# Kernel tuning notes

Hardware: AMD Instinct MI355X
Metric: run time of the kernel (lower is better)

The kernel has to match this reference:

```python
import jax, jax.numpy as jnp
import numpy as np


def cross_scan(x):
    # x: (B, D, H, W) -> xs: (B, 8, D, L)  (row, col, rev-row, rev-col, diag, antidiag, rev-diag, rev-antidiag)
    B, D, H, W = x.shape
    L = H * W
    hs = jnp.arange(H)[:, None]
    ws = jnp.arange(W)[None, :]
    x0 = x.reshape(B, D, L)                          # row-major
    x1 = jnp.swapaxes(x, 2, 3).reshape(B, D, L)      # column-major
    gd = x[:, :, hs, (hs + ws) % W]                  # diagonal gather (B,D,H,W)
    ga = x[:, :, hs, (ws - hs) % W]                  # antidiagonal gather
    x4 = jnp.swapaxes(gd, -1, -2).reshape(B, D, L)
    x5 = jnp.swapaxes(ga, -1, -2).reshape(B, D, L)
    return jnp.stack([x0, x1, x0[..., ::-1], x1[..., ::-1],
                      x4, x5, x4[..., ::-1], x5[..., ::-1]], axis=1)


def cross_merge(ys, H, W):
    # ys: (B, 8, D, L) -> (B, D, L), inverse-scatter + sum of all 8 directions
    B, K, D, L = ys.shape
    hs = jnp.arange(H)[:, None]
    ws = jnp.arange(W)[None, :]
    y = ys[:, 0] + ys[:, 2, :, ::-1]
    yt = (ys[:, 1] + ys[:, 3, :, ::-1]).reshape(B, D, W, H)
    y = y + jnp.swapaxes(yt, -1, -2).reshape(B, D, L)
    # diagonal scatter: result[h, w'] = t[h, (w'-h) % W]
    td = jnp.swapaxes((ys[:, 4] + ys[:, 6, :, ::-1]).reshape(B, D, W, H), -1, -2)
    y = y + td[:, :, hs, (ws - hs) % W].reshape(B, D, L)
    # antidiagonal scatter: result[h, w'] = t[h, (w'+h) % W]
    ta = jnp.swapaxes((ys[:, 5] + ys[:, 7, :, ::-1]).reshape(B, D, W, H), -1, -2)
    y = y + ta[:, :, hs, (ws + hs) % W].reshape(B, D, L)
    return y


def selective_scan(u, delta, A, Bs, Cs, Ds):
    # u, delta: (B, KD, L); A: (KD, N); Bs, Cs: (B, K, N, L); Ds: (KD,)
    Bb, KD, L = u.shape
    K = Bs.shape[1]
    Dh = KD // K
    N = A.shape[1]
    u_ = jnp.moveaxis(u.reshape(Bb, K, Dh, L), -1, 0)        # (L,B,K,Dh)
    d_ = jnp.moveaxis(delta.reshape(Bb, K, Dh, L), -1, 0)
    B_ = jnp.moveaxis(Bs, -1, 0)                              # (L,B,K,N)
    C_ = jnp.moveaxis(Cs, -1, 0)
    A_ = A.reshape(K, Dh, N)

    def step(h, inp):
        u_t, d_t, b_t, c_t = inp
        dA = jnp.exp(d_t[..., None] * A_)                     # (B,K,Dh,N)
        h = h * dA + (d_t * u_t)[..., None] * b_t[:, :, None, :]
        y = jnp.einsum('bkdn,bkn->bkd', h, c_t)
        return h, y

    h0 = jnp.zeros((Bb, K, Dh, N), u.dtype)
    _, ys = jax.lax.scan(step, h0, (u_, d_, B_, C_))          # ys: (L,B,K,Dh)
    ys = jnp.moveaxis(ys, 0, -1).reshape(Bb, KD, L)
    return ys + u * Ds[None, :, None]


def setup_inputs() -> dict:
    key = jax.random.key(0)
    ks = jax.random.split(key, 6)
    B, D, H, W = 2, 192, 64, 64
    K, N, R = 8, 16, 6
    x = jax.random.normal(ks[0], (B, D, H, W), jnp.float32)
    x_proj_weight = jax.random.normal(ks[1], (K, R + 2 * N, D), jnp.float32) * (1.0 / np.sqrt(D))
    dt_projs_weight = jax.random.normal(ks[2], (K, D, R), jnp.float32) * (0.1 / np.sqrt(R))
    dt_projs_bias = jax.random.normal(ks[3], (K, D), jnp.float32) * 0.1
    A_logs = jax.random.uniform(ks[4], (K * D, N), jnp.float32)
    Ds = jax.random.normal(ks[5], (K * D,), jnp.float32)
    ln_w = jnp.ones((D,), jnp.float32)
    ln_b = jnp.zeros((D,), jnp.float32)
    return {"x": x, "x_proj_weight": x_proj_weight, "dt_projs_weight": dt_projs_weight,
            "dt_projs_bias": dt_projs_bias, "A_logs": A_logs, "Ds": Ds,
            "ln_w": ln_w, "ln_b": ln_b}


def reference(x, x_proj_weight, dt_projs_weight, dt_projs_bias, A_logs, Ds, ln_w, ln_b):
    B, D, H, W = x.shape
    K = x_proj_weight.shape[0]
    N = A_logs.shape[1]
    R = dt_projs_weight.shape[2]
    L = H * W
    xs = cross_scan(x)                                            # (B,K,D,L)
    x_dbl = jnp.einsum('bkdl,kcd->bkcl', xs, x_proj_weight)       # (B,K,R+2N,L)
    dts, Bs, Cs = jnp.split(x_dbl, [R, R + N], axis=2)
    dts = jnp.einsum('bkrl,kdr->bkdl', dts, dt_projs_weight)      # (B,K,D,L)
    u = xs.reshape(B, K * D, L)
    delta = jax.nn.softplus(dts.reshape(B, K * D, L) + dt_projs_bias.reshape(1, K * D, 1))
    A = -jnp.exp(A_logs)                                          # (KD,N)
    ys = selective_scan(u, delta, A, Bs, Cs, Ds)                  # (B,KD,L)
    y = cross_merge(ys.reshape(B, K, D, L), H, W)                 # (B,D,L)
    y = jnp.swapaxes(y, 1, 2)                                     # (B,L,D)
    mu = y.mean(-1, keepdims=True)
    var = y.var(-1, keepdims=True)
    y = (y - mu) / jnp.sqrt(var + 1e-5) * ln_w + ln_b             # out_norm (LayerNorm)
    return y.reshape(B, H, W, D)
```

## Files before the change

kernel.cpp:

```cpp
#include <hip/hip_runtime.h>
#include <math.h>

#define BB   2
#define DD   192
#define LL   4096
#define KK   8
#define NN   16
#define RR   6
#define C38  38
#define CPAD 40
#define PQS  17
#define NCH  64
#define CLEN (LL / NCH)

__device__ __forceinline__ float fexp2(float x) { return __builtin_amdgcn_exp2f(x); }
__device__ __forceinline__ float flog2(float x) { return __builtin_amdgcn_logf(x); }

__device__ __forceinline__ float softplus_f(float x) {
  return fmaxf(x, 0.f) + 0.69314718f * flog2(1.f + fexp2(-1.44269504f * fabsf(x)));
}

__device__ __forceinline__ int src_index(int k, int l) {
  int ll = (k & 2) ? (LL - 1 - l) : l;
  int kb = k & 5;
  if (kb == 0) return ll;
  int h = ll & 63, w = ll >> 6;
  if (kb == 1) return (h << 6) + w;
  if (kb == 4) return (h << 6) + ((h + w) & 63);
  return (h << 6) + ((w - h) & 63);
}

__global__ __launch_bounds__(256) void transpose_x(const float* __restrict__ x,
                                                   float* __restrict__ xT) {
  __shared__ float tile[32][33];
  int b  = blockIdx.z;
  int p0 = blockIdx.x * 32;
  int d0 = blockIdx.y * 32;
  int tx = threadIdx.x, ty = threadIdx.y;
  #pragma unroll
  for (int i = 0; i < 32; i += 8)
    tile[ty + i][tx] = x[((size_t)(b * DD + d0 + ty + i)) * LL + p0 + tx];
  __syncthreads();
  #pragma unroll
  for (int i = 0; i < 32; i += 8)
    xT[((size_t)(b * LL + p0 + ty + i)) * DD + d0 + tx] = tile[tx][ty + i];
}

__global__ __launch_bounds__(256) void proj_kernel(const float* __restrict__ xT,
                                                   const float* __restrict__ W,
                                                   float* __restrict__ xdbl) {
  int k = blockIdx.y, b = blockIdx.z;
  int tx = threadIdx.x;
  int lloc = tx & 127, half = tx >> 7;
  int l = blockIdx.x * 128 + lloc;
  __shared__ __align__(16) float sm[DD * CPAD];
  for (int i = tx; i < C38 * DD; i += 256) {
    int c = i / DD, dq = i - c * DD;
    sm[dq * CPAD + c] = W[(k * C38 + c) * DD + dq];
  }
  for (int dq = tx; dq < DD; dq += 256) { sm[dq * CPAD + 38] = 0.f; sm[dq * CPAD + 39] = 0.f; }
  __syncthreads();

  int p = src_index(k, l);
  const float4* xrow4 = (const float4*)(xT + ((size_t)b * LL + p) * DD) + half * 24;
  const float* wbase = sm + half * 96 * CPAD;
  float4 acc[10];
  #pragma unroll
  for (int c = 0; c < 10; ++c) acc[c] = make_float4(0.f, 0.f, 0.f, 0.f);

  for (int d4 = 0; d4 < 24; ++d4) {
    float4 xv = xrow4[d4];
    #pragma unroll
    for (int s = 0; s < 4; ++s) {
      float xs = (s == 0) ? xv.x : (s == 1) ? xv.y : (s == 2) ? xv.z : xv.w;
      const float4* w4 = (const float4*)(wbase + (d4 * 4 + s) * CPAD);
      #pragma unroll
      for (int c = 0; c < 10; ++c) {
        float4 wv = w4[c];
        acc[c].x = fmaf(wv.x, xs, acc[c].x);
        acc[c].y = fmaf(wv.y, xs, acc[c].y);
        acc[c].z = fmaf(wv.z, xs, acc[c].z);
        acc[c].w = fmaf(wv.w, xs, acc[c].w);
      }
    }
  }
  __syncthreads();
  if (half == 1) {
    float* pr = sm + lloc * 41;
    const float* af = (const float*)acc;
    #pragma unroll
    for (int c = 0; c < 38; ++c) pr[c] = af[c];
  }
  __syncthreads();
  if (half == 0) {
    const float* pr = sm + lloc * 41;
    float* af = (float*)acc;
    #pragma unroll
    for (int c = 0; c < 38; ++c) af[c] += pr[c];
    float* orow = xdbl + ((size_t)((b * KK + k) * LL) + l) * CPAD;
    float4* o4 = (float4*)orow;
    #pragma unroll
    for (int c = 0; c < 9; ++c) o4[c] = acc[c];
    orow[36] = acc[9].x;
    orow[37] = acc[9].y;
  }
}

template <bool FINAL>
__global__ __launch_bounds__(384, 5) void scan_kernel(
    const float* __restrict__ xT, const float* __restrict__ xdbl,
    const float* __restrict__ A_logs, const float* __restrict__ dtw,
    const float* __restrict__ dtb, const float* __restrict__ Ds,
    float* __restrict__ Pq, float* __restrict__ Y) {
  const int lane = threadIdx.x;
  const int ng   = lane >> 5;
  const int dd   = threadIdx.y;
  const int bk   = blockIdx.x;
  const int chunk = blockIdx.y;
  const int b = bk >> 3, k = bk & 7;
  const int d  = dd * 32 + (lane & 31);
  const int kd = k * DD + d;
  const int ch = bk * DD + d;

  float An2[8];
  {
    const float* ap = A_logs + (size_t)kd * NN + ng * 8;
    #pragma unroll
    for (int j = 0; j < 8; ++j) An2[j] = -__expf(ap[j]) * 1.44269504f;
  }
  float wdt[RR];
  #pragma unroll
  for (int r = 0; r < RR; ++r) wdt[r] = dtw[kd * RR + r];
  const float bias = dtb[kd];
  const float dval = FINAL ? Ds[kd] : 0.f;

  float h[8];
  if constexpr (FINAL) {
    const float* h0p = Pq + ((size_t)ch * NCH + chunk) * PQS + 1 + ng * 8;
    #pragma unroll
    for (int j = 0; j < 8; ++j) h[j] = h0p[j];
  } else {
    #pragma unroll
    for (int j = 0; j < 8; ++j) h[j] = 0.f;
  }

  const int l0 = chunk * CLEN;
  const float* rowbase = xdbl + ((size_t)(bk * LL) + l0) * CPAD;
  const float* xTb = xT + (size_t)b * LL * DD + d;

  float S = 0.f;
  float sp[2], uu[2], Bv[2][8], Cv[2][8];
  int   pp[2];

  auto LOADT = [&](int t, int s) {
    const float* row = rowbase + (size_t)t * CPAD;
    const float2* r2 = (const float2*)row;
    float2 d01 = r2[0], d23 = r2[1], d45 = r2[2];
    float dts = bias;
    dts = fmaf(d01.x, wdt[0], dts);
    dts = fmaf(d01.y, wdt[1], dts);
    dts = fmaf(d23.x, wdt[2], dts);
    dts = fmaf(d23.y, wdt[3], dts);
    dts = fmaf(d45.x, wdt[4], dts);
    dts = fmaf(d45.y, wdt[5], dts);
    sp[s] = softplus_f(dts);
    const float2* bq = (const float2*)(row + 6 + ng * 8);
    #pragma unroll
    for (int j = 0; j < 4; ++j) {
      float2 v = bq[j];
      Bv[s][2 * j] = v.x; Bv[s][2 * j + 1] = v.y;
    }
    if constexpr (FINAL) {
      const float2* cq = (const float2*)(row + 22 + ng * 8);
      #pragma unroll
      for (int j = 0; j < 4; ++j) {
        float2 v = cq[j];
        Cv[s][2 * j] = v.x; Cv[s][2 * j + 1] = v.y;
      }
    }
    int p = src_index(k, l0 + t);
    pp[s] = p;
    uu[s] = xTb[(size_t)p * DD];
  };

  auto COMPUTE = [&](int s) {
    float spv = sp[s];
    float du = spv * uu[s];
    #pragma unroll
    for (int j = 0; j < 8; ++j) {
      float e = fexp2(spv * An2[j]);
      h[j] = fmaf(h[j], e, du * Bv[s][j]);
    }
    if constexpr (FINAL) {
      float y = 0.f;
      #pragma unroll
      for (int j = 0; j < 8; ++j) y = fmaf(h[j], Cv[s][j], y);
      y += __shfl_xor(y, 32, 64);
      if (ng == 0) {
        float outv = fmaf(uu[s], dval, y);
        atomicAdd(&Y[(size_t)(b * LL + pp[s]) * DD + d], outv);
      }
    } else {
      S += spv;
    }
  };

  LOADT(0, 0);
  for (int t = 0; t < CLEN; t += 2) {
    LOADT(t + 1, 1);
    COMPUTE(0);
    int t2 = (t + 2 < CLEN) ? t + 2 : CLEN - 1;
    LOADT(t2, 0);
    COMPUTE(1);
  }

  if constexpr (!FINAL) {
    float* rec = Pq + ((size_t)ch * NCH + chunk) * PQS;
    if (ng == 0) rec[0] = S;
    float* qp = rec + 1 + ng * 8;
    #pragma unroll
    for (int j = 0; j < 8; ++j) qp[j] = h[j];
  }
}

__global__ __launch_bounds__(256) void stitch_kernel(float* __restrict__ Pq,
                                                     const float* __restrict__ A_logs) {
  int lane = threadIdx.x & 63;
  int gw = (blockIdx.x * 256 + threadIdx.x) >> 6;
  int ch = gw >> 4, n = gw & 15;
  int kd = ch % (KK * DD);
  float An2 = -__expf(A_logs[(size_t)kd * NN + n]) * 1.44269504f;

  float* rec = Pq + ((size_t)ch * NCH + lane) * PQS;
  float P = fexp2(An2 * rec[0]);
  float q = rec[1 + n];

  float Pt = P, qt = q;
  #pragma unroll
  for (int off = 1; off < 64; off <<= 1) {
    float Pp = __shfl_up(Pt, off, 64);
    float qp = __shfl_up(qt, off, 64);
    if (lane >= off) { qt = fmaf(Pt, qp, qt); Pt *= Pp; }
  }
  float hx = __shfl_up(qt, 1, 64);
  if (lane == 0) hx = 0.f;
  rec[1 + n] = hx;
}

__global__ __launch_bounds__(256) void ln_kernel(const float* __restrict__ Y,
                                                 const float* __restrict__ lw,
                                                 const float* __restrict__ lb,
                                                 float* __restrict__ out) {
  int lane = threadIdx.x & 63;
  int row = blockIdx.x * 4 + (threadIdx.x >> 6);
  const float* yr = Y + (size_t)row * DD;
  float v0 = yr[lane], v1 = yr[lane + 64], v2 = yr[lane + 128];
  float s1 = v0 + v1 + v2;
  float s2 = v0 * v0 + v1 * v1 + v2 * v2;
  #pragma unroll
  for (int m = 32; m >= 1; m >>= 1) {
    s1 += __shfl_xor(s1, m, 64);
    s2 += __shfl_xor(s2, m, 64);
  }
  float mu = s1 * (1.f / DD);
  float var = s2 * (1.f / DD) - mu * mu;
  float inv = rsqrtf(var + 1e-5f);
  float* orow = out + (size_t)row * DD;
  orow[lane]       = (v0 - mu) * inv * lw[lane]       + lb[lane];
  orow[lane + 64]  = (v1 - mu) * inv * lw[lane + 64]  + lb[lane + 64];
  orow[lane + 128] = (v2 - mu) * inv * lw[lane + 128] + lb[lane + 128];
}

extern "C" void kernel_launch(void* const* d_in, const int* in_sizes, int n_in,
                              void* d_out, int out_size, void* d_ws, size_t ws_size,
                              hipStream_t stream) {
  const float* x      = (const float*)d_in[0];
  const float* xpw    = (const float*)d_in[1];
  const float* dtw    = (const float*)d_in[2];
  const float* dtb    = (const float*)d_in[3];
  const float* A_logs = (const float*)d_in[4];
  const float* Ds     = (const float*)d_in[5];
  const float* ln_w   = (const float*)d_in[6];
  const float* ln_b   = (const float*)d_in[7];
  float* out = (float*)d_out;

  float* ws   = (float*)d_ws;
  float* xT   = ws;
  float* xdbl = xT + 1572864;
  float* Y    = xdbl + 2621440;
  float* Pq   = Y + 1572864;

  hipMemsetAsync(Y, 0, 1572864 * sizeof(float), stream);
  transpose_x<<<dim3(LL / 32, DD / 32, BB), dim3(32, 8), 0, stream>>>(x, xT);
  proj_kernel<<<dim3(LL / 128, KK, BB), 256, 0, stream>>>(xT, xpw, xdbl);
  scan_kernel<false><<<dim3(BB * KK, NCH), dim3(64, 6), 0, stream>>>(
      xT, xdbl, A_logs, dtw, dtb, Ds, Pq, Y);
  stitch_kernel<<<(3072 * 16 * 64) / 256, 256, 0, stream>>>(Pq, A_logs);
  scan_kernel<true><<<dim3(BB * KK, NCH), dim3(64, 6), 0, stream>>>(
      xT, xdbl, A_logs, dtw, dtb, Ds, Pq, Y);
  ln_kernel<<<(BB * LL) / 4, 256, 0, stream>>>(Y, ln_w, ln_b, out);
}
```

Before: 252.7 us.

## Stage scan inputs and outputs in LDS and reorder xdbl columns for vector loads

The scan kernel now gathers each chunk's u values from xT into a 48KB LDS tile with coalesced float4 loads. Each step reads u from that tile instead of doing a scattered global load per timestep. Outputs are written back into the same tile and flushed after the loop as one batch of atomic adds. The projection kernel reorders the xdbl columns so B and C come first and dt sits at offset 32, which lets B, C and dt be read with aligned float4 loads. The larger LDS footprint lowers occupancy, and the occupancy hint drops from 5 to 4 blocks.

```diff
diff --git a/kernel.cpp b/kernel.cpp
--- a/kernel.cpp
+++ b/kernel.cpp
@@ -13,6 +13,7 @@
 #define NCH  64
 #define CLEN (LL / NCH)
 
+
 __device__ __forceinline__ float fexp2(float x) { return __builtin_amdgcn_exp2f(x); }
 __device__ __forceinline__ float flog2(float x) { return __builtin_amdgcn_logf(x); }
 
@@ -56,7 +57,8 @@
   __shared__ __align__(16) float sm[DD * CPAD];
   for (int i = tx; i < C38 * DD; i += 256) {
     int c = i / DD, dq = i - c * DD;
-    sm[dq * CPAD + c] = W[(k * C38 + c) * DD + dq];
+    int cp = (c < 6) ? (32 + c) : (c - 6);
+    sm[dq * CPAD + cp] = W[(k * C38 + c) * DD + dq];
   }
   for (int dq = tx; dq < DD; dq += 256) { sm[dq * CPAD + 38] = 0.f; sm[dq * CPAD + 39] = 0.f; }
   __syncthreads();
@@ -89,38 +91,49 @@
     float* pr = sm + lloc * 41;
     const float* af = (const float*)acc;
     #pragma unroll
-    for (int c = 0; c < 38; ++c) pr[c] = af[c];
+    for (int c = 0; c < 40; ++c) pr[c] = af[c];
   }
   __syncthreads();
   if (half == 0) {
     const float* pr = sm + lloc * 41;
     float* af = (float*)acc;
     #pragma unroll
-    for (int c = 0; c < 38; ++c) af[c] += pr[c];
-    float* orow = xdbl + ((size_t)((b * KK + k) * LL) + l) * CPAD;
-    float4* o4 = (float4*)orow;
-    #pragma unroll
-    for (int c = 0; c < 9; ++c) o4[c] = acc[c];
-    orow[36] = acc[9].x;
-    orow[37] = acc[9].y;
+    for (int c = 0; c < 40; ++c) af[c] += pr[c];
+    float4* o4 = (float4*)(xdbl + ((size_t)((b * KK + k) * LL) + l) * CPAD);
+    #pragma unroll
+    for (int c = 0; c < 10; ++c) o4[c] = acc[c];
   }
 }
 
 template <bool FINAL>
-__global__ __launch_bounds__(384, 5) void scan_kernel(
+__global__ __launch_bounds__(384, 4) void scan_kernel(
     const float* __restrict__ xT, const float* __restrict__ xdbl,
     const float* __restrict__ A_logs, const float* __restrict__ dtw,
     const float* __restrict__ dtb, const float* __restrict__ Ds,
     float* __restrict__ Pq, float* __restrict__ Y) {
+  __shared__ float utile[CLEN * DD];
+  __shared__ int ptab[CLEN];
   const int lane = threadIdx.x;
   const int ng   = lane >> 5;
   const int dd   = threadIdx.y;
+  const int tid  = dd * 64 + lane;
   const int bk   = blockIdx.x;
   const int chunk = blockIdx.y;
   const int b = bk >> 3, k = bk & 7;
   const int d  = dd * 32 + (lane & 31);
   const int kd = k * DD + d;
   const int ch = bk * DD + d;
+  const int l0 = chunk * CLEN;
+
+  const float* xTb_base = xT + (size_t)b * LL * DD;
+  if (tid < CLEN) ptab[tid] = src_index(k, l0 + tid);
+  #pragma unroll
+  for (int i = 0; i < 8; ++i) {
+    int idx = tid + 384 * i;
+    int t = idx / 48, c4 = idx - t * 48;
+    int p = src_index(k, l0 + t);
+    ((float4*)utile)[idx] = ((const float4*)(xTb_base + (size_t)p * DD))[c4];
+  }
 
   float An2[8];
   {
@@ -144,46 +157,39 @@
     for (int j = 0; j < 8; ++j) h[j] = 0.f;
   }
 
-  const int l0 = chunk * CLEN;
   const float* rowbase = xdbl + ((size_t)(bk * LL) + l0) * CPAD;
-  const float* xTb = xT + (size_t)b * LL * DD + d;
 
   float S = 0.f;
   float sp[2], uu[2], Bv[2][8], Cv[2][8];
-  int   pp[2];
+
+  __syncthreads();
 
   auto LOADT = [&](int t, int s) {
     const float* row = rowbase + (size_t)t * CPAD;
-    const float2* r2 = (const float2*)row;
-    float2 d01 = r2[0], d23 = r2[1], d45 = r2[2];
+    const float4* b4 = (const float4*)row + ng * 2;
+    float4 bv0 = b4[0], bv1 = b4[1];
+    Bv[s][0] = bv0.x; Bv[s][1] = bv0.y; Bv[s][2] = bv0.z; Bv[s][3] = bv0.w;
+    Bv[s][4] = bv1.x; Bv[s][5] = bv1.y; Bv[s][6] = bv1.z; Bv[s][7] = bv1.w;
+    if constexpr (FINAL) {
+      const float4* c4 = (const float4*)(row + 16) + ng * 2;
+      float4 cv0 = c4[0], cv1 = c4[1];
+      Cv[s][0] = cv0.x; Cv[s][1] = cv0.y; Cv[s][2] = cv0.z; Cv[s][3] = cv0.w;
+      Cv[s][4] = cv1.x; Cv[s][5] = cv1.y; Cv[s][6] = cv1.z; Cv[s][7] = cv1.w;
+    }
+    float4 dt4 = *(const float4*)(row + 32);
+    float2 dt2 = *(const float2*)(row + 36);
     float dts = bias;
-    dts = fmaf(d01.x, wdt[0], dts);
-    dts = fmaf(d01.y, wdt[1], dts);
-    dts = fmaf(d23.x, wdt[2], dts);
-    dts = fmaf(d23.y, wdt[3], dts);
-    dts = fmaf(d45.x, wdt[4], dts);
-    dts = fmaf(d45.y, wdt[5], dts);
+    dts = fmaf(dt4.x, wdt[0], dts);
+    dts = fmaf(dt4.y, wdt[1], dts);
+    dts = fmaf(dt4.z, wdt[2], dts);
+    dts = fmaf(dt4.w, wdt[3], dts);
+    dts = fmaf(dt2.x, wdt[4], dts);
+    dts = fmaf(dt2.y, wdt[5], dts);
     sp[s] = softplus_f(dts);
-    const float2* bq = (const float2*)(row + 6 + ng * 8);
-    #pragma unroll
-    for (int j = 0; j < 4; ++j) {
-      float2 v = bq[j];
-      Bv[s][2 * j] = v.x; Bv[s][2 * j + 1] = v.y;
-    }
-    if constexpr (FINAL) {
-      const float2* cq = (const float2*)(row + 22 + ng * 8);
-      #pragma unroll
-      for (int j = 0; j < 4; ++j) {
-        float2 v = cq[j];
-        Cv[s][2 * j] = v.x; Cv[s][2 * j + 1] = v.y;
-      }
-    }
-    int p = src_index(k, l0 + t);
-    pp[s] = p;
-    uu[s] = xTb[(size_t)p * DD];
+    uu[s] = utile[t * DD + d];
   };
 
-  auto COMPUTE = [&](int s) {
+  auto COMPUTE = [&](int t, int s) {
     float spv = sp[s];
     float du = spv * uu[s];
     #pragma unroll
@@ -196,10 +202,7 @@
       #pragma unroll
       for (int j = 0; j < 8; ++j) y = fmaf(h[j], Cv[s][j], y);
       y += __shfl_xor(y, 32, 64);
-      if (ng == 0) {
-        float outv = fmaf(uu[s], dval, y);
-        atomicAdd(&Y[(size_t)(b * LL + pp[s]) * DD + d], outv);
-      }
+      if (ng == 0) utile[t * DD + d] = fmaf(uu[s], dval, y);
     } else {
       S += spv;
     }
@@ -208,15 +211,24 @@
   LOADT(0, 0);
   for (int t = 0; t < CLEN; t += 2) {
     LOADT(t + 1, 1);
-    COMPUTE(0);
+    COMPUTE(t, 0);
     int t2 = (t + 2 < CLEN) ? t + 2 : CLEN - 1;
     LOADT(t2, 0);
-    COMPUTE(1);
-  }
-
-  if constexpr (!FINAL) {
+    COMPUTE(t + 1, 1);
+  }
+
+  if constexpr (FINAL) {
+    __syncthreads();
+    float* Yb = Y + (size_t)b * LL * DD;
+    #pragma unroll
+    for (int i = 0; i < 32; ++i) {
+      int idx = tid + 384 * i;
+      int t = idx / DD, dcol = idx - t * DD;
+      atomicAdd(&Yb[(size_t)ptab[t] * DD + dcol], utile[idx]);
+    }
+  } else {
     float* rec = Pq + ((size_t)ch * NCH + chunk) * PQS;
-    if (ng == 0) rec[0] = S;
+    if (ng == 0 && dd < 6) rec[0] = S;
     float* qp = rec + 1 + ng * 8;
     #pragma unroll
     for (int j = 0; j < 8; ++j) qp[j] = h[j];
```

After: 292.5 us. 15.8% more time.
